# Performance work log

Measured on AMD Instinct MI355X. Metric: run time of the kernel, lower is better.

The kernel has to match this reference:

```python
import jax, jax.numpy as jnp
import numpy as np

B, T, IN, H, NH = 64, 512, 1024, 1024, 4
HD = H // NH  # head_dim = 256
NG = 3        # gates: z (update), r (reset), n (candidate)


def setup_inputs() -> dict:
    key = jax.random.key(0)
    k1, k2, k3, k4, k5 = jax.random.split(key, 5)
    inp = jax.random.normal(k1, (B, T, IN), dtype=jnp.float32)
    # nn.Linear(input_size, 3*hidden_size): weight [3H, IN], bias [3H]
    W = jax.random.normal(k2, (IN, NG * H), dtype=jnp.float32) / np.sqrt(IN)
    bW = jax.random.normal(k3, (NG * H,), dtype=jnp.float32) * 0.02
    # recurrent R: [num_heads, head_dim_in, num_gates, head_dim_out], std=1/sqrt(head_dim)
    R = jax.random.normal(k4, (NH, HD, NG, HD), dtype=jnp.float32) / np.sqrt(HD)
    b = jax.random.normal(k5, (NH, NG, HD), dtype=jnp.float32)
    return {"input": inp, "W": W, "bW": bW, "R": R, "b": b}


def _gru_scan(Wx, R, b, h0):
    # Wx: [T, B, NH, NG, HD], h0: [B, NH, HD]
    def step(h, wx):
        # recurrent gate preactivations: Ry[b,h,g,o] = sum_i h[b,h,i] R[h,i,g,o]
        ry = jnp.einsum('bhi,higo->bhgo', h, R)
        z = jax.nn.sigmoid(wx[:, :, 0] + ry[:, :, 0] + b[:, 0])
        r = jax.nn.sigmoid(wx[:, :, 1] + ry[:, :, 1] + b[:, 1])
        n = jnp.tanh(wx[:, :, 2] + r * ry[:, :, 2] + b[:, 2])
        h_new = z * h + (1.0 - z) * n
        return h_new, h_new

    h_last, hs = jax.lax.scan(step, h0, Wx)
    return hs, h_last  # hs: [T, B, NH, HD]


def reference(input, W, bW, R, b):
    bs, sl = input.shape[0], input.shape[1]
    # input projection for all timesteps at once
    Wx = input @ W + bW                               # [B, T, NG*H]
    Wx = Wx.reshape(bs, sl, NG, NH, HD)
    Wx = jnp.transpose(Wx, (1, 0, 3, 2, 4))           # [T, B, NH, NG, HD]
    h0 = jnp.zeros((bs, NH, HD), dtype=input.dtype)
    hs, h_last = _gru_scan(Wx, R, b, h0)
    h = jnp.transpose(hs, (1, 0, 2, 3)).reshape(bs, sl, H)   # [B, T, H]
    hn = h_last.reshape(1, bs, H)                             # [num_layers=1, B, H]
    return h, hn
```

## Files before the change

kernel.cpp:

```cpp
#include <hip/hip_runtime.h>
#include <hip/hip_fp16.h>


typedef _Float16 f16x8 __attribute__((ext_vector_type(8)));
typedef float    f32x4 __attribute__((ext_vector_type(4)));

#define AS1 __attribute__((address_space(1)))
#define AS3 __attribute__((address_space(3)))

__device__ __forceinline__ void async_ld16(const void* g, void* l) {
    __builtin_amdgcn_global_load_lds((const AS1 void*)g, (AS3 void*)l, 16, 0, 0);
}

__device__ __forceinline__ float sigmoidf_(float x) {
    return 1.f / (1.f + __expf(-x));
}
__device__ __forceinline__ float tanhf_(float x) {
    float e = __expf(-2.f * fabsf(x));
    float r = (1.f - e) / (1.f + e);
    return copysignf(r, x);
}

__global__ __launch_bounds__(256) void cast_to_f16(const float* __restrict__ in,
                                                   _Float16* __restrict__ out, int n8) {
    int i = blockIdx.x * 256 + threadIdx.x;
    if (i >= n8) return;
    const float4* p = (const float4*)in;
    float4 a = p[2 * i], b = p[2 * i + 1];
    f16x8 r;
    r[0] = (_Float16)a.x; r[1] = (_Float16)a.y; r[2] = (_Float16)a.z; r[3] = (_Float16)a.w;
    r[4] = (_Float16)b.x; r[5] = (_Float16)b.y; r[6] = (_Float16)b.z; r[7] = (_Float16)b.w;
    *(f16x8*)(out + (size_t)i * 8) = r;
}

__global__ __launch_bounds__(256) void transpose_cast(const float* __restrict__ W,
                                                      _Float16* __restrict__ WT) {
    __shared__ float tile[32][33];
    const int tx = threadIdx.x, ty = threadIdx.y;
    const int n0 = blockIdx.x * 32, k0 = blockIdx.y * 32;
#pragma unroll
    for (int j = 0; j < 32; j += 8)
        tile[ty + j][tx] = W[(size_t)(k0 + ty + j) * 3072 + n0 + tx];
    __syncthreads();
#pragma unroll
    for (int j = 0; j < 32; j += 8)
        WT[(size_t)(n0 + ty + j) * 1024 + k0 + tx] = (_Float16)tile[tx][ty + j];
}

__global__ __launch_bounds__(256) void gemm_wx(const _Float16* __restrict__ A,
                                               const _Float16* __restrict__ BT,
                                               const float* __restrict__ bW,
                                               const float* __restrict__ bR,
                                               float* __restrict__ Wx) {
    __shared__ _Float16 As[128 * 32];
    __shared__ _Float16 Bs[128 * 32];
    const int tid  = threadIdx.x;
    const int wave = tid >> 6, lane = tid & 63;
    const int m0 = blockIdx.y * 128, n0 = blockIdx.x * 128;
    const int wm = (wave >> 1) * 64, wn = (wave & 1) * 64;
    const int r16 = lane & 15, kq = lane >> 4;

    f32x4 acc[4][4];
#pragma unroll
    for (int m = 0; m < 4; m++)
#pragma unroll
        for (int n = 0; n < 4; n++) acc[m][n] = (f32x4){0.f, 0.f, 0.f, 0.f};

    const int srow = wave * 32 + (lane >> 2);
    const int scol = (lane & 3) * 8;

    for (int kt = 0; kt < 32; kt++) {
        const int k0 = kt * 32;
#pragma unroll
        for (int j = 0; j < 2; j++) {
            async_ld16(A  + (size_t)(m0 + srow + j * 16) * 1024 + k0 + scol,
                       As + (wave * 32 + j * 16) * 32);
            async_ld16(BT + (size_t)(n0 + srow + j * 16) * 1024 + k0 + scol,
                       Bs + (wave * 32 + j * 16) * 32);
        }
        __syncthreads();
        f16x8 af[4], bf[4];
#pragma unroll
        for (int m = 0; m < 4; m++) af[m] = *(const f16x8*)(As + (wm + m * 16 + r16) * 32 + kq * 8);
#pragma unroll
        for (int n = 0; n < 4; n++) bf[n] = *(const f16x8*)(Bs + (wn + n * 16 + r16) * 32 + kq * 8);
#pragma unroll
        for (int m = 0; m < 4; m++)
#pragma unroll
            for (int n = 0; n < 4; n++)
                acc[m][n] = __builtin_amdgcn_mfma_f32_16x16x32_f16(af[m], bf[n], acc[m][n], 0, 0, 0);
        __syncthreads();
    }

#pragma unroll
    for (int m = 0; m < 4; m++) {
        const int row0 = m0 + wm + m * 16 + (lane >> 4) * 4;
#pragma unroll
        for (int n = 0; n < 4; n++) {
            const int col  = n0 + wn + n * 16 + r16;
            const int g    = col >> 10, head = (col >> 8) & 3, o = col & 255;
            const float bias = bW[col] + bR[head * 768 + g * 256 + o];
#pragma unroll
            for (int q = 0; q < 4; q++) {
                const int rr = row0 + q;
                const int t = rr & 511, bb = rr >> 9;
                Wx[(((size_t)t * 64 + bb) * 12 + head * 3 + g) * 256 + o] = acc[m][n][q] + bias;
            }
        }
    }
}

__global__ __launch_bounds__(512) void scan_mfma(const float* __restrict__ R,
                                                 const float* __restrict__ Wx,
                                                 float* __restrict__ out) {
    __shared__ _Float16 Rbuf[3 * 256 * 40];
    __shared__ _Float16 h16[2 * 256];

    const int bx = blockIdx.x;
    const int head = bx >> 6, b = bx & 63;
    const int t0 = threadIdx.x;
    const int w = t0 >> 6, l = t0 & 63;
    const int c = l & 15, kq = l >> 4;
    const int o0 = w * 32;

    f16x8 Bf[3][2][7];
#pragma unroll
    for (int kt = 0; kt < 8; kt++) {
        __syncthreads();
        for (int idx = t0; idx < 32 * 768; idx += 512) {
            const int i2 = idx >> 8 >> 1 >> 0;
            const int ii = idx / 768;
            const int rem = idx - ii * 768;
            const int g = rem >> 8, o = rem & 255;
            Rbuf[(g * 256 + o) * 40 + ii] =
                (_Float16)R[(((size_t)head * 256 + kt * 32 + ii) * 3 + g) * 256 + o];
            (void)i2;
        }
        __syncthreads();
        if (kt < 7) {
#pragma unroll
            for (int g = 0; g < 3; g++)
#pragma unroll
                for (int ot = 0; ot < 2; ot++)
                    Bf[g][ot][kt] =
                        *(const f16x8*)(Rbuf + ((size_t)(g * 256 + o0 + ot * 16 + c)) * 40 + kq * 8);
        }
    }

    if (t0 < 512) { h16[t0] = (_Float16)0.f; }

    float hprev[2] = {0.f, 0.f};
    float wxc[3][2];
#pragma unroll
    for (int g = 0; g < 3; g++)
#pragma unroll
        for (int o2 = 0; o2 < 2; o2++)
            wxc[g][o2] = Wx[(((size_t)0 * 64 + b) * 12 + head * 3 + g) * 256 + o0 + o2 * 16 + c];
    __syncthreads();

    float* outb = out + ((size_t)b * 512) * 1024 + head * 256;
    int cur = 0;

    for (int t = 0; t < 512; t++) {
        f32x4 acc[3][2];
#pragma unroll
        for (int g = 0; g < 3; g++)
#pragma unroll
            for (int ot = 0; ot < 2; ot++) acc[g][ot] = (f32x4){0.f, 0.f, 0.f, 0.f};

#pragma unroll
        for (int kt = 0; kt < 7; kt++) {
            const f16x8 Af = *(const f16x8*)(h16 + cur * 256 + kt * 32 + kq * 8);
#pragma unroll
            for (int g = 0; g < 3; g++)
#pragma unroll
                for (int ot = 0; ot < 2; ot++)
                    acc[g][ot] = __builtin_amdgcn_mfma_f32_16x16x32_f16(Af, Bf[g][ot][kt],
                                                                        acc[g][ot], 0, 0, 0);
        }
        {
            const f16x8 Af = *(const f16x8*)(h16 + cur * 256 + 7 * 32 + kq * 8);
#pragma unroll
            for (int g = 0; g < 3; g++)
#pragma unroll
                for (int ot = 0; ot < 2; ot++) {
                    const f16x8 Bs =
                        *(const f16x8*)(Rbuf + ((size_t)(g * 256 + o0 + ot * 16 + c)) * 40 + kq * 8);
                    acc[g][ot] = __builtin_amdgcn_mfma_f32_16x16x32_f16(Af, Bs,
                                                                        acc[g][ot], 0, 0, 0);
                }
        }

        float wxn[3][2];
        if (t < 511) {
#pragma unroll
            for (int g = 0; g < 3; g++)
#pragma unroll
                for (int o2 = 0; o2 < 2; o2++)
                    wxn[g][o2] = Wx[(((size_t)(t + 1) * 64 + b) * 12 + head * 3 + g) * 256 +
                                    o0 + o2 * 16 + c];
        } else {
            wxn[0][0] = wxn[0][1] = wxn[1][0] = wxn[1][1] = wxn[2][0] = wxn[2][1] = 0.f;
        }

#pragma unroll
        for (int o2 = 0; o2 < 2; o2++) {
            const float z = sigmoidf_(wxc[0][o2] + acc[0][o2][0]);
            const float r = sigmoidf_(wxc[1][o2] + acc[1][o2][0]);
            const float n = tanhf_(wxc[2][o2] + r * acc[2][o2][0]);
            const float h = z * hprev[o2] + (1.f - z) * n;
            hprev[o2] = h;
            if (kq == 0) {
                outb[(size_t)t * 1024 + o0 + o2 * 16 + c] = h;
                h16[(cur ^ 1) * 256 + o0 + o2 * 16 + c] = (_Float16)h;
            }
        }
#pragma unroll
        for (int g = 0; g < 3; g++)
#pragma unroll
            for (int o2 = 0; o2 < 2; o2++) wxc[g][o2] = wxn[g][o2];

        __syncthreads();
        cur ^= 1;
    }
}

__global__ __launch_bounds__(256) void copy_hn(float* __restrict__ out) {
    const int idx = blockIdx.x * 256 + threadIdx.x;
    out[(size_t)64 * 512 * 1024 + idx] =
        out[((size_t)(idx >> 10) * 512 + 511) * 1024 + (idx & 1023)];
}

extern "C" void kernel_launch(void* const* d_in, const int* in_sizes, int n_in,
                              void* d_out, int out_size, void* d_ws, size_t ws_size,
                              hipStream_t stream) {
    (void)in_sizes; (void)n_in; (void)out_size; (void)ws_size;
    const float* inp = (const float*)d_in[0];
    const float* W   = (const float*)d_in[1];
    const float* bW  = (const float*)d_in[2];
    const float* R   = (const float*)d_in[3];
    const float* bR  = (const float*)d_in[4];
    float* out = (float*)d_out;

    _Float16* A16 = (_Float16*)d_ws;
    _Float16* WT  = (_Float16*)((char*)d_ws + 67108864);
    float*    Wx  = (float*)((char*)d_ws + 73400320);

    cast_to_f16<<<16384, 256, 0, stream>>>(inp, A16, 4194304);
    transpose_cast<<<dim3(96, 32), dim3(32, 8), 0, stream>>>(W, WT);
    gemm_wx<<<dim3(24, 256), 256, 0, stream>>>(A16, WT, bW, bR, Wx);
    scan_mfma<<<256, 512, 0, stream>>>(R, Wx, out);
    copy_hn<<<256, 256, 0, stream>>>(out);
}
```

Baseline: 1.057 ms.

## Prefetch h fragments in scan loop, use fast reciprocal, fuse hn copy

The recurrent scan loop now preloads the last R slice and the first h fragment from LDS and software-pipelines the h fragment loads one k-step ahead of the MFMAs. The Wx prefetch for the next step is issued before the MFMA chain. Sigmoid and tanh use a hardware reciprocal instead of division, and the final-state output is written directly by the scan kernel, which removes the separate copy_hn launch. The aim is to shorten the serial per-timestep latency and drop one kernel launch. The trade-off is a slightly less accurate reciprocal and more registers held live.

```diff
diff --git a/kernel.cpp b/kernel.cpp
--- a/kernel.cpp
+++ b/kernel.cpp
@@ -12,12 +12,21 @@
     __builtin_amdgcn_global_load_lds((const AS1 void*)g, (AS3 void*)l, 16, 0, 0);
 }
 
+#if defined(__has_builtin)
+#if __has_builtin(__builtin_amdgcn_rcpf)
+#define RCPF(x) __builtin_amdgcn_rcpf(x)
+#endif
+#endif
+#ifndef RCPF
+#define RCPF(x) (1.f / (x))
+#endif
+
 __device__ __forceinline__ float sigmoidf_(float x) {
-    return 1.f / (1.f + __expf(-x));
+    return RCPF(1.f + __expf(-x));
 }
 __device__ __forceinline__ float tanhf_(float x) {
     float e = __expf(-2.f * fabsf(x));
-    float r = (1.f - e) / (1.f + e);
+    float r = (1.f - e) * RCPF(1.f + e);
     return copysignf(r, x);
 }
 
@@ -128,13 +137,11 @@
     for (int kt = 0; kt < 8; kt++) {
         __syncthreads();
         for (int idx = t0; idx < 32 * 768; idx += 512) {
-            const int i2 = idx >> 8 >> 1 >> 0;
             const int ii = idx / 768;
             const int rem = idx - ii * 768;
             const int g = rem >> 8, o = rem & 255;
             Rbuf[(g * 256 + o) * 40 + ii] =
                 (_Float16)R[(((size_t)head * 256 + kt * 32 + ii) * 3 + g) * 256 + o];
-            (void)i2;
         }
         __syncthreads();
         if (kt < 7) {
@@ -147,9 +154,12 @@
         }
     }
 
-    if (t0 < 512) { h16[t0] = (_Float16)0.f; }
+    h16[t0] = (_Float16)0.f;
 
     float hprev[2] = {0.f, 0.f};
+    float* outb = out + ((size_t)b * 512) * 1024 + head * 256;
+    float* hnp  = out + (size_t)64 * 512 * 1024 + b * 1024 + head * 256;
+
     float wxc[3][2];
 #pragma unroll
     for (int g = 0; g < 3; g++)
@@ -158,38 +168,18 @@
             wxc[g][o2] = Wx[(((size_t)0 * 64 + b) * 12 + head * 3 + g) * 256 + o0 + o2 * 16 + c];
     __syncthreads();
 
-    float* outb = out + ((size_t)b * 512) * 1024 + head * 256;
     int cur = 0;
-
     for (int t = 0; t < 512; t++) {
-        f32x4 acc[3][2];
+        const _Float16* hc = h16 + cur * 256;
+
+        f16x8 Bs7[3][2];
 #pragma unroll
         for (int g = 0; g < 3; g++)
 #pragma unroll
-            for (int ot = 0; ot < 2; ot++) acc[g][ot] = (f32x4){0.f, 0.f, 0.f, 0.f};
-
-#pragma unroll
-        for (int kt = 0; kt < 7; kt++) {
-            const f16x8 Af = *(const f16x8*)(h16 + cur * 256 + kt * 32 + kq * 8);
-#pragma unroll
-            for (int g = 0; g < 3; g++)
-#pragma unroll
-                for (int ot = 0; ot < 2; ot++)
-                    acc[g][ot] = __builtin_amdgcn_mfma_f32_16x16x32_f16(Af, Bf[g][ot][kt],
-                                                                        acc[g][ot], 0, 0, 0);
-        }
-        {
-            const f16x8 Af = *(const f16x8*)(h16 + cur * 256 + 7 * 32 + kq * 8);
-#pragma unroll
-            for (int g = 0; g < 3; g++)
-#pragma unroll
-                for (int ot = 0; ot < 2; ot++) {
-                    const f16x8 Bs =
-                        *(const f16x8*)(Rbuf + ((size_t)(g * 256 + o0 + ot * 16 + c)) * 40 + kq * 8);
-                    acc[g][ot] = __builtin_amdgcn_mfma_f32_16x16x32_f16(Af, Bs,
-                                                                        acc[g][ot], 0, 0, 0);
-                }
-        }
+            for (int ot = 0; ot < 2; ot++)
+                Bs7[g][ot] =
+                    *(const f16x8*)(Rbuf + ((size_t)(g * 256 + o0 + ot * 16 + c)) * 40 + kq * 8);
+        f16x8 Af0 = *(const f16x8*)(hc + 0 * 32 + kq * 8);
 
         float wxn[3][2];
         if (t < 511) {
@@ -203,16 +193,36 @@
             wxn[0][0] = wxn[0][1] = wxn[1][0] = wxn[1][1] = wxn[2][0] = wxn[2][1] = 0.f;
         }
 
+        f32x4 acc[3][2];
+#pragma unroll
+        for (int g = 0; g < 3; g++)
+#pragma unroll
+            for (int ot = 0; ot < 2; ot++) acc[g][ot] = (f32x4){0.f, 0.f, 0.f, 0.f};
+
+#pragma unroll
+        for (int kt = 0; kt < 8; kt++) {
+            f16x8 Af1;
+            if (kt < 7) Af1 = *(const f16x8*)(hc + (kt + 1) * 32 + kq * 8);
+#pragma unroll
+            for (int g = 0; g < 3; g++)
+#pragma unroll
+                for (int ot = 0; ot < 2; ot++)
+                    acc[g][ot] = __builtin_amdgcn_mfma_f32_16x16x32_f16(
+                        Af0, (kt < 7) ? Bf[g][ot][kt] : Bs7[g][ot], acc[g][ot], 0, 0, 0);
+            Af0 = Af1;
+        }
+
+        _Float16* hw = h16 + (cur ^ 1) * 256;
 #pragma unroll
         for (int o2 = 0; o2 < 2; o2++) {
             const float z = sigmoidf_(wxc[0][o2] + acc[0][o2][0]);
             const float r = sigmoidf_(wxc[1][o2] + acc[1][o2][0]);
             const float n = tanhf_(wxc[2][o2] + r * acc[2][o2][0]);
-            const float h = z * hprev[o2] + (1.f - z) * n;
+            const float h = n + z * (hprev[o2] - n);
             hprev[o2] = h;
             if (kq == 0) {
                 outb[(size_t)t * 1024 + o0 + o2 * 16 + c] = h;
-                h16[(cur ^ 1) * 256 + o0 + o2 * 16 + c] = (_Float16)h;
+                hw[o0 + o2 * 16 + c] = (_Float16)h;
             }
         }
 #pragma unroll
@@ -223,12 +233,10 @@
         __syncthreads();
         cur ^= 1;
     }
-}
-
-__global__ __launch_bounds__(256) void copy_hn(float* __restrict__ out) {
-    const int idx = blockIdx.x * 256 + threadIdx.x;
-    out[(size_t)64 * 512 * 1024 + idx] =
-        out[((size_t)(idx >> 10) * 512 + 511) * 1024 + (idx & 1023)];
+    if (kq == 0) {
+#pragma unroll
+        for (int o2 = 0; o2 < 2; o2++) hnp[o0 + o2 * 16 + c] = hprev[o2];
+    }
 }
 
 extern "C" void kernel_launch(void* const* d_in, const int* in_sizes, int n_in,
@@ -250,5 +258,4 @@
     transpose_cast<<<dim3(96, 32), dim3(32, 8), 0, stream>>>(W, WT);
     gemm_wx<<<dim3(24, 256), 256, 0, stream>>>(A16, WT, bW, bR, Wx);
     scan_mfma<<<256, 512, 0, stream>>>(R, Wx, out);
-    copy_hn<<<256, 256, 0, stream>>>(out);
-}
+}
```

After: 1.073 ms. Within noise of the previous version (+1.5%).
